# Performance work log

Measured on AMD Instinct MI355X. Metric: run time of the kernel, lower is better.

The kernel has to match this reference:

```python
import jax, jax.numpy as jnp
import numpy as np

B, P, M, W = 32, 4096, 12, 9
IN_C, OUT_C = 64, 64
IN_PN_PAD = P + 1  # in_point_num + 1 padding row


def setup_inputs() -> dict:
    key = jax.random.key(0)
    k1, k2, k3, k4 = jax.random.split(key, 4)
    in_pc_pad = jax.random.normal(k1, (B, IN_PN_PAD, IN_C), dtype=jnp.float32)
    weights = jax.random.normal(k2, (W, OUT_C * IN_C), dtype=jnp.float32)
    bias = jnp.zeros((OUT_C,), dtype=jnp.float32)
    w_weights = jax.random.normal(k3, (P, M, W), dtype=jnp.float32) / (9.0 * W)
    neighbor_id_lstlst = jax.random.randint(k4, (P, M), 0, IN_PN_PAD, dtype=jnp.int64)
    neighbor_mask_lst = jnp.ones((P, M), dtype=jnp.float32)
    return {
        "in_pc_pad": in_pc_pad,
        "weights": weights,
        "bias": bias,
        "w_weights": w_weights,
        "neighbor_id_lstlst": neighbor_id_lstlst,
        "neighbor_mask_lst": neighbor_mask_lst,
    }


def reference(in_pc_pad, weights, bias, w_weights, neighbor_id_lstlst, neighbor_mask_lst):
    # gather neighbor features: [B, P, M, IN_C]
    in_neighbors = in_pc_pad[:, neighbor_id_lstlst]
    # mask the per-(point,neighbor) basis coefficients: [P, M, W]
    w2 = w_weights * neighbor_mask_lst[:, :, None]
    # synthesize per-(point,neighbor) weight matrices from basis: [P, M, OUT_C, IN_C]
    wmat = jnp.einsum('pmw,wc->pmc', w2, weights).reshape(P, M, OUT_C, IN_C)
    # batched matvec + neighbor-sum reduce (fused over m): [B, P, OUT_C]
    out_pc = jnp.einsum('pmoi,bpmi->bpo', wmat, in_neighbors)
    return out_pc + bias
```

## Files before the change

kernel.cpp:

```cpp
#include <hip/hip_runtime.h>
#include <hip/hip_bf16.h>

#define NB 32
#define NP 4096
#define NM 12
#define NW 9
#define NC 64
#define PN_PAD 4097
#define KDIM (NW * NC)
#define KSTEPS (KDIM / 32)
#define AROW 584

typedef __attribute__((ext_vector_type(8))) short short8;
typedef __attribute__((ext_vector_type(4))) float float4v;

__device__ __forceinline__ unsigned short f32_to_bf16(float f) {
    union { float f; unsigned u; } v; v.f = f;
    unsigned r = v.u + 0x7FFFu + ((v.u >> 16) & 1u);
    return (unsigned short)(r >> 16);
}

__global__ void prep_weights(const float* __restrict__ w,
                             unsigned short* __restrict__ wsw) {
    int idx = blockIdx.x * 256 + threadIdx.x;
    if (idx >= KDIM * NC) return;
    int j    = idx & 7;
    int lane = (idx >> 3) & 63;
    int nt   = (idx >> 9) & 3;
    int ks   = idx >> 11;
    int k = ks * 32 + ((lane >> 4) * 8) + j;
    int n = nt * 16 + (lane & 15);
    int wi = k >> 6;
    int ii = k & 63;
    wsw[idx] = f32_to_bf16(w[wi * (NC * NC) + n * NC + ii]);
}

__global__ __launch_bounds__(256)
void conv_main(const float* __restrict__ x,
               const unsigned short* __restrict__ wsw,
               const float* __restrict__ bias,
               const float* __restrict__ ww,
               const int* __restrict__ nid,
               const float* __restrict__ mask,
               float* __restrict__ out)
{
    __shared__ __align__(16) unsigned short A[NB * AROW];
    __shared__ float s_w2[NM * NW];
    __shared__ int s_nid[NM];

    const int p = blockIdx.x;
    const int tid = threadIdx.x;

    if (tid < NM * NW) s_w2[tid] = ww[p * (NM * NW) + tid] * mask[p * NM + tid / NW];
    if (tid < NM) s_nid[tid] = nid[p * NM + tid];
    __syncthreads();

    {
        const int i  = tid & 63;
        const int b0 = tid >> 6;
        float acc[8][9];
        #pragma unroll
        for (int it = 0; it < 8; ++it)
            #pragma unroll
            for (int w = 0; w < 9; ++w) acc[it][w] = 0.f;

        #pragma unroll 1
        for (int m = 0; m < NM; ++m) {
            const int nm = s_nid[m];
            float wv[9];
            #pragma unroll
            for (int w = 0; w < 9; ++w) wv[w] = s_w2[m * NW + w];
            float xv[8];
            #pragma unroll
            for (int it = 0; it < 8; ++it) {
                const int b = b0 + it * 4;
                xv[it] = x[(b * PN_PAD + nm) * NC + i];
            }
            #pragma unroll
            for (int it = 0; it < 8; ++it)
                #pragma unroll
                for (int w = 0; w < 9; ++w)
                    acc[it][w] = fmaf(wv[w], xv[it], acc[it][w]);
        }

        #pragma unroll
        for (int it = 0; it < 8; ++it) {
            const int b = b0 + it * 4;
            #pragma unroll
            for (int w = 0; w < 9; ++w)
                A[b * AROW + w * 64 + i] = f32_to_bf16(acc[it][w]);
        }
    }
    __syncthreads();

    {
        const int lane = tid & 63;
        const int nt   = tid >> 6;
        const int quad = lane >> 4;
        const int l15  = lane & 15;

        float4v acc0 = {0.f, 0.f, 0.f, 0.f};
        float4v acc1 = {0.f, 0.f, 0.f, 0.f};
        const short8* Bfrags = (const short8*)wsw;

        #pragma unroll
        for (int ks = 0; ks < KSTEPS; ++ks) {
            short8 bfrag = Bfrags[(ks * 4 + nt) * 64 + lane];
            const short8 a0 = *(const short8*)&A[(l15     ) * AROW + ks * 32 + quad * 8];
            const short8 a1 = *(const short8*)&A[(16 + l15) * AROW + ks * 32 + quad * 8];
            acc0 = __builtin_amdgcn_mfma_f32_16x16x32_bf16(a0, bfrag, acc0, 0, 0, 0);
            acc1 = __builtin_amdgcn_mfma_f32_16x16x32_bf16(a1, bfrag, acc1, 0, 0, 0);
        }

        const int o = nt * 16 + l15;
        const float bv = bias[o];
        #pragma unroll
        for (int reg = 0; reg < 4; ++reg) {
            const int r0 = quad * 4 + reg;
            out[(r0 * NP + p) * NC + o] = acc0[reg] + bv;
            const int r1 = 16 + r0;
            out[(r1 * NP + p) * NC + o] = acc1[reg] + bv;
        }
    }
}

extern "C" void kernel_launch(void* const* d_in, const int* in_sizes, int n_in,
                              void* d_out, int out_size, void* d_ws, size_t ws_size,
                              hipStream_t stream) {
    const float* x    = (const float*)d_in[0];
    const float* w    = (const float*)d_in[1];
    const float* bias = (const float*)d_in[2];
    const float* ww   = (const float*)d_in[3];
    const int*   nid  = (const int*)d_in[4];
    const float* mask = (const float*)d_in[5];
    float* out = (float*)d_out;
    unsigned short* wsw = (unsigned short*)d_ws;

    hipLaunchKernelGGL(prep_weights, dim3((KDIM * NC + 255) / 256), dim3(256), 0, stream,
                       w, wsw);
    hipLaunchKernelGGL(conv_main, dim3(NP), dim3(256), 0, stream,
                       x, wsw, bias, ww, nid, mask, out);
}
```

Measured before the change: 146.7 us.

## Vectorize neighbor gather with float4 loads and precompute masked basis coefficients

The gather phase now has each thread load float4 vectors for two batch rows instead of eight scalar loads, and packs the bf16 results into 8-byte LDS stores. The masked basis coefficients are precomputed by the prep kernel into a padded workspace array, which removes the shared-memory staging and the first barrier in the main kernel. The bf16 packing now uses simple round-half-up instead of round-to-nearest-even, which changes rounding slightly. The coefficient and neighbor-index reads are now per-thread global loads that rely on the cache.

```diff
diff --git a/kernel.cpp b/kernel.cpp
--- a/kernel.cpp
+++ b/kernel.cpp
@@ -11,6 +11,9 @@
 #define KSTEPS (KDIM / 32)
 #define AROW 584
 
+#define WSW_BYTES (KDIM * NC * 2)
+#define W2_OFFSET WSW_BYTES
+
 typedef __attribute__((ext_vector_type(8))) short short8;
 typedef __attribute__((ext_vector_type(4))) float float4v;
 
@@ -20,75 +23,88 @@
     return (unsigned short)(r >> 16);
 }
 
-__global__ void prep_weights(const float* __restrict__ w,
-                             unsigned short* __restrict__ wsw) {
+__device__ __forceinline__ uint2 pack_bf16x4(float4v v) {
+    union { float f; unsigned u; } a0, a1, a2, a3;
+    a0.f = v[0]; a1.f = v[1]; a2.f = v[2]; a3.f = v[3];
+    unsigned u0 = a0.u + 0x8000u, u1 = a1.u + 0x8000u;
+    unsigned u2 = a2.u + 0x8000u, u3 = a3.u + 0x8000u;
+    uint2 r;
+    r.x = __builtin_amdgcn_perm(u1, u0, 0x07060302u);
+    r.y = __builtin_amdgcn_perm(u3, u2, 0x07060302u);
+    return r;
+}
+
+__global__ void prep(const float* __restrict__ w,
+                     const float* __restrict__ ww,
+                     const float* __restrict__ mask,
+                     unsigned short* __restrict__ wsw,
+                     float* __restrict__ w2d) {
     int idx = blockIdx.x * 256 + threadIdx.x;
-    if (idx >= KDIM * NC) return;
-    int j    = idx & 7;
-    int lane = (idx >> 3) & 63;
-    int nt   = (idx >> 9) & 3;
-    int ks   = idx >> 11;
-    int k = ks * 32 + ((lane >> 4) * 8) + j;
-    int n = nt * 16 + (lane & 15);
-    int wi = k >> 6;
-    int ii = k & 63;
-    wsw[idx] = f32_to_bf16(w[wi * (NC * NC) + n * NC + ii]);
+    if (idx < KDIM * NC) {
+        int j    = idx & 7;
+        int lane = (idx >> 3) & 63;
+        int nt   = (idx >> 9) & 3;
+        int ks   = idx >> 11;
+        int k = ks * 32 + ((lane >> 4) * 8) + j;
+        int n = nt * 16 + (lane & 15);
+        int wi = k >> 6;
+        int ii = k & 63;
+        wsw[idx] = f32_to_bf16(w[wi * (NC * NC) + n * NC + ii]);
+    }
+    if (idx < NP * NM * NW) {
+        int wq = idx % NW;
+        int pm = idx / NW;
+        w2d[pm * 12 + wq] = ww[idx] * mask[pm];
+    }
 }
 
 __global__ __launch_bounds__(256)
 void conv_main(const float* __restrict__ x,
                const unsigned short* __restrict__ wsw,
                const float* __restrict__ bias,
-               const float* __restrict__ ww,
+               const float* __restrict__ w2d,
                const int* __restrict__ nid,
-               const float* __restrict__ mask,
                float* __restrict__ out)
 {
     __shared__ __align__(16) unsigned short A[NB * AROW];
-    __shared__ float s_w2[NM * NW];
-    __shared__ int s_nid[NM];
 
     const int p = blockIdx.x;
     const int tid = threadIdx.x;
 
-    if (tid < NM * NW) s_w2[tid] = ww[p * (NM * NW) + tid] * mask[p * NM + tid / NW];
-    if (tid < NM) s_nid[tid] = nid[p * NM + tid];
-    __syncthreads();
+    {
+        const int i4 = tid & 15;
+        const int bs = tid >> 4;
+        const float4v* x4 = (const float4v*)x;
+        const float* w2p = w2d + p * (NM * 12);
+        const int* nidp = nid + p * NM;
 
-    {
-        const int i  = tid & 63;
-        const int b0 = tid >> 6;
-        float acc[8][9];
+        int nm[NM];
         #pragma unroll
-        for (int it = 0; it < 8; ++it)
+        for (int m = 0; m < NM; ++m) nm[m] = nidp[m];
+
+        float4v acc0[NW], acc1[NW];
+        #pragma unroll
+        for (int w = 0; w < NW; ++w) {
+            acc0[w] = (float4v){0.f, 0.f, 0.f, 0.f};
+            acc1[w] = (float4v){0.f, 0.f, 0.f, 0.f};
+        }
+
+        #pragma unroll 2
+        for (int m = 0; m < NM; ++m) {
+            const float4v xv0 = x4[(bs * PN_PAD + nm[m]) * 16 + i4];
+            const float4v xv1 = x4[((bs + 16) * PN_PAD + nm[m]) * 16 + i4];
             #pragma unroll
-            for (int w = 0; w < 9; ++w) acc[it][w] = 0.f;
-
-        #pragma unroll 1
-        for (int m = 0; m < NM; ++m) {
-            const int nm = s_nid[m];
-            float wv[9];
-            #pragma unroll
-            for (int w = 0; w < 9; ++w) wv[w] = s_w2[m * NW + w];
-            float xv[8];
-            #pragma unroll
-            for (int it = 0; it < 8; ++it) {
-                const int b = b0 + it * 4;
-                xv[it] = x[(b * PN_PAD + nm) * NC + i];
+            for (int w = 0; w < NW; ++w) {
+                const float wv = w2p[m * 12 + w];
+                acc0[w] += wv * xv0;
+                acc1[w] += wv * xv1;
             }
-            #pragma unroll
-            for (int it = 0; it < 8; ++it)
-                #pragma unroll
-                for (int w = 0; w < 9; ++w)
-                    acc[it][w] = fmaf(wv[w], xv[it], acc[it][w]);
         }
 
         #pragma unroll
-        for (int it = 0; it < 8; ++it) {
-            const int b = b0 + it * 4;
-            #pragma unroll
-            for (int w = 0; w < 9; ++w)
-                A[b * AROW + w * 64 + i] = f32_to_bf16(acc[it][w]);
+        for (int w = 0; w < NW; ++w) {
+            *(uint2*)&A[bs * AROW + w * 64 + i4 * 4] = pack_bf16x4(acc0[w]);
+            *(uint2*)&A[(bs + 16) * AROW + w * 64 + i4 * 4] = pack_bf16x4(acc1[w]);
         }
     }
     __syncthreads();
@@ -135,9 +151,11 @@
     const float* mask = (const float*)d_in[5];
     float* out = (float*)d_out;
     unsigned short* wsw = (unsigned short*)d_ws;
+    float* w2d = (float*)((char*)d_ws + W2_OFFSET);
 
-    hipLaunchKernelGGL(prep_weights, dim3((KDIM * NC + 255) / 256), dim3(256), 0, stream,
-                       w, wsw);
+    const int prep_elems = NP * NM * NW;
+    hipLaunchKernelGGL(prep, dim3((prep_elems + 255) / 256), dim3(256), 0, stream,
+                       w, ww, mask, wsw, w2d);
     hipLaunchKernelGGL(conv_main, dim3(NP), dim3(256), 0, stream,
-                       x, wsw, bias, ww, nid, mask, out);
+                       x, wsw, bias, w2d, nid, out);
 }
```

Measured after the change: 144.9 us. No clear change (-1.2%).
